# Kernel optimization log

Hardware: AMD Instinct MI355X
Metric: run time of the kernel (lower is better)

Reference implementation:

```python
import jax, jax.numpy as jnp
import numpy as np

# CSC-FC connectivity constants (match init_kwargs)
C = 8192   # input features (csc_c)
N = 8192   # output features (csc_n)
F = 64     # fan-in per output neuron (csc_f)
S = 1      # stride of connectivity window (csc_s)
B = 128    # batch

# Precompute gather indices: output neuron j connects to inputs (j*S + k) % C, k in [0, F)
_IDX = (np.arange(N, dtype=np.int32)[:, None] * S + np.arange(F, dtype=np.int32)[None, :]) % C  # [N, F]


def setup_inputs() -> dict:
    key = jax.random.key(0)
    k1, k2 = jax.random.split(key)
    x = jax.random.normal(k1, (B, C), dtype=jnp.float32)
    kernel = jax.random.normal(k2, (C, N), dtype=jnp.float32) * 0.05
    bias = jnp.zeros((N,), dtype=jnp.float32)
    return {"x": x, "kernel": kernel, "bias": bias}


def reference(x, kernel, bias):
    idx = jnp.asarray(_IDX)                      # [N, F] int32
    cols = jnp.arange(N, dtype=jnp.int32)[:, None]
    w_g = kernel[idx, cols]                      # [N, F] gathered sparse weights
    x_g = x[:, idx]                              # [B, N, F] gathered inputs
    # out[b, n] = sum_f x_g[b, n, f] * w_g[n, f] + bias[n]
    return jnp.einsum('bnf,nf->bn', x_g, w_g) + bias
```

## Files before the change

kernel.cpp:

```cpp
#include <hip/hip_runtime.h>

#define C_DIM 8192
#define N_DIM 8192
#define B_DIM 128
#define TN 128
#define TB 16
#define XW 260
#define WS 132

typedef float f4 __attribute__((ext_vector_type(4)));

__global__ __launch_bounds__(256) void cscfc_kernel(
    const float* __restrict__ x,
    const float* __restrict__ K,
    const float* __restrict__ bias,
    float* __restrict__ out)
{
    __shared__ float x_s[TB * XW];
    __shared__ float w_t[64 * WS];

    const int t    = threadIdx.x;
    const int lane = t & 63;
    const int rg   = t >> 6;
    const int n0   = blockIdx.x * TN;
    const int b0   = blockIdx.y * TB;

    f4 xq[4];
    #pragma unroll
    for (int i = 0; i < 4; ++i) {
        const int g   = t + 256 * i;
        const int row = g >> 6;
        const int col = (g & 63) * 4;
        xq[i] = *(const f4*)&x[(size_t)(b0 + row) * C_DIM + ((n0 + col) & (C_DIM - 1))];
    }

    f4 kq[16];
    int krow[16], kcol[16];
    #pragma unroll
    for (int i = 0; i < 16; ++i) {
        const int g = t + 256 * i;
        int rr, qc;
        if (g < 1024)      { rr = g >> 4;                    qc = g & 15; }
        else if (g < 3072) { const int h = g - 1024; rr = 64 + (h >> 5); qc = h & 31; }
        else               { const int h = g - 3072; rr = 128 + (h >> 4); qc = 16 + (h & 15); }
        krow[i] = rr;
        kcol[i] = qc * 4;
        const int c = (n0 + rr) & (C_DIM - 1);
        kq[i] = *(const f4*)&K[(size_t)c * N_DIM + n0 + qc * 4];
    }

    #pragma unroll
    for (int i = 0; i < 4; ++i) {
        const int g   = t + 256 * i;
        const int row = g >> 6;
        const int col = (g & 63) * 4;
        *(f4*)&x_s[row * XW + col] = xq[i];
    }
    #pragma unroll
    for (int i = 0; i < 16; ++i) {
        #pragma unroll
        for (int k = 0; k < 4; ++k) {
            const int n_loc = kcol[i] + k;
            const int f     = krow[i] - n_loc;
            if ((unsigned)f < 64u) w_t[f * WS + n_loc] = kq[i][k];
        }
    }
    __syncthreads();

    const int ng     = lane & 31;
    const int n_base = ng * 4;
    const int bg     = (lane >> 5) | (rg << 1);
    const int bl0    = bg;
    const int bl1    = bg + 8;

    float acc0[4] = {0.f, 0.f, 0.f, 0.f};
    float acc1[4] = {0.f, 0.f, 0.f, 0.f};

    #pragma unroll 4
    for (int f0 = 0; f0 < 64; f0 += 4) {
        const f4 w0 = *(const f4*)&w_t[(f0 + 0) * WS + n_base];
        const f4 w1 = *(const f4*)&w_t[(f0 + 1) * WS + n_base];
        const f4 w2 = *(const f4*)&w_t[(f0 + 2) * WS + n_base];
        const f4 w3 = *(const f4*)&w_t[(f0 + 3) * WS + n_base];

        const float* xs0 = &x_s[bl0 * XW + n_base + f0];
        const f4 xa = *(const f4*)(xs0);
        const f4 xb = *(const f4*)(xs0 + 4);
        acc0[0] = fmaf(xa.x, w0.x, fmaf(xa.y, w1.x, fmaf(xa.z, w2.x, fmaf(xa.w, w3.x, acc0[0]))));
        acc0[1] = fmaf(xa.y, w0.y, fmaf(xa.z, w1.y, fmaf(xa.w, w2.y, fmaf(xb.x, w3.y, acc0[1]))));
        acc0[2] = fmaf(xa.z, w0.z, fmaf(xa.w, w1.z, fmaf(xb.x, w2.z, fmaf(xb.y, w3.z, acc0[2]))));
        acc0[3] = fmaf(xa.w, w0.w, fmaf(xb.x, w1.w, fmaf(xb.y, w2.w, fmaf(xb.z, w3.w, acc0[3]))));

        const float* xs1 = &x_s[bl1 * XW + n_base + f0];
        const f4 xc = *(const f4*)(xs1);
        const f4 xd = *(const f4*)(xs1 + 4);
        acc1[0] = fmaf(xc.x, w0.x, fmaf(xc.y, w1.x, fmaf(xc.z, w2.x, fmaf(xc.w, w3.x, acc1[0]))));
        acc1[1] = fmaf(xc.y, w0.y, fmaf(xc.z, w1.y, fmaf(xc.w, w2.y, fmaf(xd.x, w3.y, acc1[1]))));
        acc1[2] = fmaf(xc.z, w0.z, fmaf(xc.w, w1.z, fmaf(xd.x, w2.z, fmaf(xd.y, w3.z, acc1[2]))));
        acc1[3] = fmaf(xc.w, w0.w, fmaf(xd.x, w1.w, fmaf(xd.y, w2.w, fmaf(xd.z, w3.w, acc1[3]))));
    }

    const f4 bv = *(const f4*)(bias + n0 + n_base);
    f4 o0, o1;
    o0.x = acc0[0] + bv.x; o0.y = acc0[1] + bv.y; o0.z = acc0[2] + bv.z; o0.w = acc0[3] + bv.w;
    o1.x = acc1[0] + bv.x; o1.y = acc1[1] + bv.y; o1.z = acc1[2] + bv.z; o1.w = acc1[3] + bv.w;
    *(f4*)(out + (size_t)(b0 + bl0) * N_DIM + n0 + n_base) = o0;
    *(f4*)(out + (size_t)(b0 + bl1) * N_DIM + n0 + n_base) = o1;
}

extern "C" void kernel_launch(void* const* d_in, const int* in_sizes, int n_in,
                              void* d_out, int out_size, void* d_ws, size_t ws_size,
                              hipStream_t stream) {
    const float* x    = (const float*)d_in[0];
    const float* K    = (const float*)d_in[1];
    const float* bias = (const float*)d_in[2];
    float* out = (float*)d_out;

    dim3 grid(N_DIM / TN, B_DIM / TB, 1);
    dim3 block(256, 1, 1);
    cscfc_kernel<<<grid, block, 0, stream>>>(x, K, bias, out);
}
```

Before: 301.0 us.

## Stream x directly from global memory with register sliding window instead of LDS

Removes the shared-memory staging of the x tile and instead has each thread load its x values straight from global memory, keeping a two-vector sliding window in registers across the fully unrolled f loop. The scatter of weights into LDS now becomes branchless, with out-of-band entries written to an extra dummy row. This cuts LDS traffic and the x store before the barrier, but adds many small global loads per thread that depend on cache hits, since x rows are reused across blocks.

```diff
diff --git a/kernel.cpp b/kernel.cpp
--- a/kernel.cpp
+++ b/kernel.cpp
@@ -5,10 +5,13 @@
 #define B_DIM 128
 #define TN 128
 #define TB 16
-#define XW 260
 #define WS 132
 
 typedef float f4 __attribute__((ext_vector_type(4)));
+
+__device__ __forceinline__ f4 ldx(const float* __restrict__ xr, int c) {
+    return *(const f4*)&xr[c & (C_DIM - 1)];
+}
 
 __global__ __launch_bounds__(256) void cscfc_kernel(
     const float* __restrict__ x,
@@ -16,23 +19,13 @@
     const float* __restrict__ bias,
     float* __restrict__ out)
 {
-    __shared__ float x_s[TB * XW];
-    __shared__ float w_t[64 * WS];
+    __shared__ float w_t[65 * WS];
 
     const int t    = threadIdx.x;
     const int lane = t & 63;
     const int rg   = t >> 6;
     const int n0   = blockIdx.x * TN;
     const int b0   = blockIdx.y * TB;
-
-    f4 xq[4];
-    #pragma unroll
-    for (int i = 0; i < 4; ++i) {
-        const int g   = t + 256 * i;
-        const int row = g >> 6;
-        const int col = (g & 63) * 4;
-        xq[i] = *(const f4*)&x[(size_t)(b0 + row) * C_DIM + ((n0 + col) & (C_DIM - 1))];
-    }
 
     f4 kq[16];
     int krow[16], kcol[16];
@@ -50,19 +43,13 @@
     }
 
     #pragma unroll
-    for (int i = 0; i < 4; ++i) {
-        const int g   = t + 256 * i;
-        const int row = g >> 6;
-        const int col = (g & 63) * 4;
-        *(f4*)&x_s[row * XW + col] = xq[i];
-    }
-    #pragma unroll
     for (int i = 0; i < 16; ++i) {
         #pragma unroll
         for (int k = 0; k < 4; ++k) {
             const int n_loc = kcol[i] + k;
             const int f     = krow[i] - n_loc;
-            if ((unsigned)f < 64u) w_t[f * WS + n_loc] = kq[i][k];
+            const int fc    = ((unsigned)f < 64u) ? f : 64;
+            w_t[fc * WS + n_loc] = kq[i][k];
         }
     }
     __syncthreads();
@@ -73,31 +60,39 @@
     const int bl0    = bg;
     const int bl1    = bg + 8;
 
+    const float* __restrict__ xr0 = x + (size_t)(b0 + bl0) * C_DIM;
+    const float* __restrict__ xr1 = x + (size_t)(b0 + bl1) * C_DIM;
+    const int cbase = n0 + n_base;
+
     float acc0[4] = {0.f, 0.f, 0.f, 0.f};
     float acc1[4] = {0.f, 0.f, 0.f, 0.f};
 
-    #pragma unroll 4
+    f4 xcur0 = ldx(xr0, cbase);
+    f4 xnxt0 = ldx(xr0, cbase + 4);
+    f4 xcur1 = ldx(xr1, cbase);
+    f4 xnxt1 = ldx(xr1, cbase + 4);
+
+    #pragma unroll
     for (int f0 = 0; f0 < 64; f0 += 4) {
         const f4 w0 = *(const f4*)&w_t[(f0 + 0) * WS + n_base];
         const f4 w1 = *(const f4*)&w_t[(f0 + 1) * WS + n_base];
         const f4 w2 = *(const f4*)&w_t[(f0 + 2) * WS + n_base];
         const f4 w3 = *(const f4*)&w_t[(f0 + 3) * WS + n_base];
 
-        const float* xs0 = &x_s[bl0 * XW + n_base + f0];
-        const f4 xa = *(const f4*)(xs0);
-        const f4 xb = *(const f4*)(xs0 + 4);
-        acc0[0] = fmaf(xa.x, w0.x, fmaf(xa.y, w1.x, fmaf(xa.z, w2.x, fmaf(xa.w, w3.x, acc0[0]))));
-        acc0[1] = fmaf(xa.y, w0.y, fmaf(xa.z, w1.y, fmaf(xa.w, w2.y, fmaf(xb.x, w3.y, acc0[1]))));
-        acc0[2] = fmaf(xa.z, w0.z, fmaf(xa.w, w1.z, fmaf(xb.x, w2.z, fmaf(xb.y, w3.z, acc0[2]))));
-        acc0[3] = fmaf(xa.w, w0.w, fmaf(xb.x, w1.w, fmaf(xb.y, w2.w, fmaf(xb.z, w3.w, acc0[3]))));
+        acc0[0] = fmaf(xcur0.x, w0.x, fmaf(xcur0.y, w1.x, fmaf(xcur0.z, w2.x, fmaf(xcur0.w, w3.x, acc0[0]))));
+        acc0[1] = fmaf(xcur0.y, w0.y, fmaf(xcur0.z, w1.y, fmaf(xcur0.w, w2.y, fmaf(xnxt0.x, w3.y, acc0[1]))));
+        acc0[2] = fmaf(xcur0.z, w0.z, fmaf(xcur0.w, w1.z, fmaf(xnxt0.x, w2.z, fmaf(xnxt0.y, w3.z, acc0[2]))));
+        acc0[3] = fmaf(xcur0.w, w0.w, fmaf(xnxt0.x, w1.w, fmaf(xnxt0.y, w2.w, fmaf(xnxt0.z, w3.w, acc0[3]))));
 
-        const float* xs1 = &x_s[bl1 * XW + n_base + f0];
-        const f4 xc = *(const f4*)(xs1);
-        const f4 xd = *(const f4*)(xs1 + 4);
-        acc1[0] = fmaf(xc.x, w0.x, fmaf(xc.y, w1.x, fmaf(xc.z, w2.x, fmaf(xc.w, w3.x, acc1[0]))));
-        acc1[1] = fmaf(xc.y, w0.y, fmaf(xc.z, w1.y, fmaf(xc.w, w2.y, fmaf(xd.x, w3.y, acc1[1]))));
-        acc1[2] = fmaf(xc.z, w0.z, fmaf(xc.w, w1.z, fmaf(xd.x, w2.z, fmaf(xd.y, w3.z, acc1[2]))));
-        acc1[3] = fmaf(xc.w, w0.w, fmaf(xd.x, w1.w, fmaf(xd.y, w2.w, fmaf(xd.z, w3.w, acc1[3]))));
+        acc1[0] = fmaf(xcur1.x, w0.x, fmaf(xcur1.y, w1.x, fmaf(xcur1.z, w2.x, fmaf(xcur1.w, w3.x, acc1[0]))));
+        acc1[1] = fmaf(xcur1.y, w0.y, fmaf(xcur1.z, w1.y, fmaf(xcur1.w, w2.y, fmaf(xnxt1.x, w3.y, acc1[1]))));
+        acc1[2] = fmaf(xcur1.z, w0.z, fmaf(xcur1.w, w1.z, fmaf(xnxt1.x, w2.z, fmaf(xnxt1.y, w3.z, acc1[2]))));
+        acc1[3] = fmaf(xcur1.w, w0.w, fmaf(xnxt1.x, w1.w, fmaf(xnxt1.y, w2.w, fmaf(xnxt1.z, w3.w, acc1[3]))));
+
+        if (f0 < 60) {
+            xcur0 = xnxt0;  xnxt0 = ldx(xr0, cbase + f0 + 8);
+            xcur1 = xnxt1;  xnxt1 = ldx(xr1, cbase + f0 + 8);
+        }
     }
 
     const f4 bv = *(const f4*)(bias + n0 + n_base);
```

Measured after the change: 299.8 us. About the same (-0.4%).
